# Kernel optimization log

Measured on AMD Instinct MI355X. Metric: run time of the kernel, lower is better.

Reference implementation:

```python
import jax, jax.numpy as jnp
import numpy as np

E = 1024      # embed_dim
QH = 16       # query heads
KVH = 4       # kv heads
HD = E // QH  # head_dim = 64
KVE = HD * KVH  # 256
EPS = 1e-5
ROPE_BASE = 10000.0


def rope(x, d):
    # Faithful to the source RoPE: d == number of heads (x.shape[-2]),
    # and the 'sequence' axis of the cache is x.shape[0] (the batch dim).
    # rope(x) = x*cos + (x*sin) * neg_half(x)  (note: nonlinear in x).
    b = x.shape[0]
    theta = 1.0 / (ROPE_BASE ** (jnp.arange(0, d, 2, dtype=jnp.float32) / d))  # (d//2,)
    seq_idx = jnp.arange(b, dtype=jnp.float32)                                 # (b,)
    idx_theta = seq_idx[:, None] * theta[None, :]                              # (b, d//2)
    idx2 = jnp.concatenate([idx_theta, idx_theta], axis=-1)                    # (b, d)
    # cached shape (b,1,1,d); source permutes (0,1,3,2) -> (b,1,d,1)
    cos = jnp.cos(idx2)[:, None, :, None]  # (b,1,d,1)
    sin = jnp.sin(idx2)[:, None, :, None]
    d2 = d // 2
    # split of the LAST dim (head_dim) at d//2 == num_heads//2, as in source
    neg = jnp.concatenate([-x[..., d2:], x[..., :d2]], axis=-1)
    return x * cos + (x * sin) * neg


def setup_inputs() -> dict:
    key = jax.random.key(0)
    ks = jax.random.split(key, 12)
    b, n = 1, 2048

    def xavier(k, shape):
        fan_out, fan_in = shape
        std = (2.0 / (fan_in + fan_out)) ** 0.5
        return jax.random.normal(k, shape, dtype=jnp.float32) * std

    return {
        "query": jax.random.normal(ks[0], (b, n, E), dtype=jnp.float32),
        "key": jax.random.normal(ks[1], (b, n, E), dtype=jnp.float32),
        "value": jax.random.normal(ks[2], (b, n, E), dtype=jnp.float32),
        "Wq": xavier(ks[3], (E, E)),
        "bq": jnp.zeros((E,), jnp.float32),
        "Wk": xavier(ks[4], (KVE, E)),
        "bk": jnp.zeros((KVE,), jnp.float32),
        "Wv": xavier(ks[5], (KVE, E)),
        "bv": jnp.zeros((KVE,), jnp.float32),
        "gamma": jnp.ones((E,), jnp.float32),
        "beta": jnp.zeros((E,), jnp.float32),
    }


def reference(query, key, value, Wq, bq, Wk, bk, Wv, bv, gamma, beta):
    b, n, _ = query.shape
    q = query @ Wq.T + bq            # (b,n,E)
    k = key @ Wk.T + bk              # (b,n,KVE)
    v = value @ Wv.T + bv            # (b,n,KVE)

    q = q.reshape(b, n, QH, HD)      # b n h d
    k = k.reshape(b, n, KVH, HD)
    v = v.reshape(b, n, KVH, HD)

    q = rope(q, QH)
    k = rope(k, KVH)

    # b n h d -> b h n d
    q = jnp.transpose(q, (0, 2, 1, 3))
    k = jnp.transpose(k, (0, 2, 1, 3))
    v = jnp.transpose(v, (0, 2, 1, 3))

    scale = float(HD) ** 0.5
    q = q / scale

    g = QH // KVH
    # 'b (h g) n d -> b g h n d' : h outer, g inner
    q = q.reshape(b, KVH, g, n, HD)              # (b, h, g, n, d)
    q = jnp.transpose(q, (0, 2, 1, 3, 4))        # (b, g, h, n, d)

    sim = jnp.einsum('bghnd,bhsd->bghns', q, k)  # (b,g,h,n,s)
    attn = jax.nn.softmax(sim, axis=-1)
    out = jnp.einsum('bghns,bhsd->bghnd', attn, v)

    # 'b g h n d -> b n (h g) d'
    out = jnp.transpose(out, (0, 3, 2, 1, 4))    # (b, n, h, g, d)
    x = out.reshape(b, n, QH * HD)               # (b, n, E)

    # LayerNorm (biased variance, as in torch)
    mu = jnp.mean(x, axis=-1, keepdims=True)
    var = jnp.mean((x - mu) ** 2, axis=-1, keepdims=True)
    x = (x - mu) * jax.lax.rsqrt(var + EPS) * gamma + beta

    # NOTE: source computes out_proj(x) but returns x, so out_proj is dead code.
    return x
```

## Files before the change

kernel.cpp:

```cpp
#include <hip/hip_runtime.h>
#include <math.h>

#define EDIM   1024
#define KVEDIM 256
#define HDIM   64
#define QHEADS 16

typedef __attribute__((ext_vector_type(8))) short short8;
typedef __attribute__((ext_vector_type(4))) float f32x4;

__device__ __forceinline__ short f2b(float a) {
    unsigned ua = __builtin_bit_cast(unsigned, a);
    ua += 0x7fffu + ((ua >> 16) & 1u);
    return (short)(ua >> 16);
}
__device__ __forceinline__ unsigned cvtpk(float a, float b) {
    unsigned r;
    asm("v_cvt_pk_bf16_f32 %0, %1, %2" : "=v"(r) : "v"(a), "v"(b));
    return r;
}

__global__ __launch_bounds__(256)
void proj_gemm(const float* __restrict__ Aq, const float* __restrict__ Ak,
               const float* __restrict__ Av,
               const float* __restrict__ Wqf, const float* __restrict__ Wkf,
               const float* __restrict__ Wvf,
               const float* __restrict__ bq, const float* __restrict__ bk,
               const float* __restrict__ bv,
               short* __restrict__ Cq, short* __restrict__ Ck,
               short* __restrict__ Cv, float qscale, int n)
{
    const int bid = blockIdx.x;
    const float* A; const float* W; const float* bias; short* C;
    int N, bm, bn; float scale; int vtrans;
    if (bid < 512) {
        A = Aq; W = Wqf; bias = bq; C = Cq; N = EDIM; scale = qscale; vtrans = 0;
        bm = (bid >> 4) * 64; bn = (bid & 15) * 64;
    } else if (bid < 640) {
        int i = bid - 512;
        A = Ak; W = Wkf; bias = bk; C = Ck; N = KVEDIM; scale = 1.0f; vtrans = 0;
        bm = (i >> 2) * 64; bn = (i & 3) * 64;
    } else {
        int i = bid - 640;
        A = Av; W = Wvf; bias = bv; C = Cv; N = KVEDIM; scale = 1.0f; vtrans = 1;
        bm = (i >> 2) * 64; bn = (i & 3) * 64;
    }
    const int K = EDIM;

    __shared__ short As[64 * 72];
    __shared__ short Ws[64 * 72];

    const int t = threadIdx.x, lane = t & 63, wv = t >> 6;
    const int lm = lane & 15, quad = lane >> 4;
    const int q8 = quad * 8, q4 = quad * 4;
    const int wm = (wv & 1) * 32, wn = (wv >> 1) * 32;
    const int sr = t >> 2, c0 = (t & 3) * 16;

    const f32x4 zero = {0.f, 0.f, 0.f, 0.f};
    f32x4 acc[2][2] = {{zero, zero}, {zero, zero}};

    for (int k0 = 0; k0 < K; k0 += 64) {
        __syncthreads();
        {
            const float4* ap = (const float4*)&A[(size_t)(bm + sr) * K + k0 + c0];
            float4 a0 = ap[0], a1 = ap[1], a2 = ap[2], a3 = ap[3];
            uint4 o0, o1;
            o0.x = cvtpk(a0.x, a0.y); o0.y = cvtpk(a0.z, a0.w);
            o0.z = cvtpk(a1.x, a1.y); o0.w = cvtpk(a1.z, a1.w);
            o1.x = cvtpk(a2.x, a2.y); o1.y = cvtpk(a2.z, a2.w);
            o1.z = cvtpk(a3.x, a3.y); o1.w = cvtpk(a3.z, a3.w);
            *(uint4*)&As[sr * 72 + c0]     = o0;
            *(uint4*)&As[sr * 72 + c0 + 8] = o1;
            const float4* wp = (const float4*)&W[(size_t)(bn + sr) * K + k0 + c0];
            float4 w0 = wp[0], w1 = wp[1], w2 = wp[2], w3 = wp[3];
            uint4 p0, p1;
            p0.x = cvtpk(w0.x, w0.y); p0.y = cvtpk(w0.z, w0.w);
            p0.z = cvtpk(w1.x, w1.y); p0.w = cvtpk(w1.z, w1.w);
            p1.x = cvtpk(w2.x, w2.y); p1.y = cvtpk(w2.z, w2.w);
            p1.z = cvtpk(w3.x, w3.y); p1.w = cvtpk(w3.z, w3.w);
            *(uint4*)&Ws[sr * 72 + c0]     = p0;
            *(uint4*)&Ws[sr * 72 + c0 + 8] = p1;
        }
        __syncthreads();
        #pragma unroll
        for (int ks = 0; ks < 2; ++ks) {
            short8 af[2], bfr[2];
            #pragma unroll
            for (int i = 0; i < 2; ++i)
                af[i] = *(const short8*)&As[(wm + i * 16 + lm) * 72 + ks * 32 + q8];
            #pragma unroll
            for (int j = 0; j < 2; ++j)
                bfr[j] = *(const short8*)&Ws[(wn + j * 16 + lm) * 72 + ks * 32 + q8];
            #pragma unroll
            for (int i = 0; i < 2; ++i)
                #pragma unroll
                for (int j = 0; j < 2; ++j)
                    acc[i][j] = __builtin_amdgcn_mfma_f32_16x16x32_bf16(
                        af[i], bfr[j], acc[i][j], 0, 0, 0);
        }
    }

    if (!vtrans) {
        #pragma unroll
        for (int j = 0; j < 2; ++j) {
            float bj = bias[bn + wn + j * 16 + lm];
            #pragma unroll
            for (int i = 0; i < 2; ++i)
                #pragma unroll
                for (int r = 0; r < 4; ++r)
                    C[(size_t)(bm + wm + i * 16 + q4 + r) * N + bn + wn + j * 16 + lm] =
                        f2b((acc[i][j][r] + bj) * scale);
        }
    } else {
        #pragma unroll
        for (int j = 0; j < 2; ++j) {
            float bj = bias[bn + wn + j * 16 + lm];
            const size_t drow = (size_t)(bn + wn + j * 16 + lm) * n;
            #pragma unroll
            for (int i = 0; i < 2; ++i) {
                uint2 o;
                o.x = cvtpk(acc[i][j][0] + bj, acc[i][j][1] + bj);
                o.y = cvtpk(acc[i][j][2] + bj, acc[i][j][3] + bj);
                *(uint2*)&C[drow + bm + wm + i * 16 + q4] = o;
            }
        }
    }
}

__global__ __launch_bounds__(256, 4)
void attn_mfma(const short* __restrict__ q, const short* __restrict__ k,
               const short* __restrict__ vt, float* __restrict__ x,
               float* __restrict__ opart, float* __restrict__ lpart,
               int n, int s_len, int partial)
{
    __shared__ short Ks[64 * 64];
    __shared__ short Vs[4096];

    const int kvh = blockIdx.y;
    const int r0  = blockIdx.x * 16;
    const int t = threadIdx.x, lane = t & 63, wv = t >> 6;
    const int qh = (kvh << 2) | wv;
    const int lm = lane & 15, quad = lane >> 4, q8 = quad * 8;

    short8 qf0, qf1;
    {
        const short* qp = &q[(size_t)(r0 + lm) * EDIM + qh * HDIM];
        qf0 = *(const short8*)&qp[q8];
        qf1 = *(const short8*)&qp[32 + q8];
    }

    const f32x4 zero = {0.f, 0.f, 0.f, 0.f};
    f32x4 oacc[4] = {zero, zero, zero, zero};
    float lp = 0.f;

    const int sr  = t >> 2;
    const int scs = (t & 3) * 16;
    const int swS = (sr & 7) << 3;
    const int kw0 = sr * 64 + (scs ^ swS);
    const int kw1 = sr * 64 + ((scs + 8) ^ swS);
    const int krx  = q8 ^ ((lm & 7) << 3);
    const int krx2 = (32 + q8) ^ ((lm & 7) << 3);

    const int vd = t >> 2, vc = t & 3;
    const int vktp = vc >> 1, vhalf = vc & 1;
    int vsx[4];
    #pragma unroll
    for (int p = 0; p < 4; ++p) {
        int slot = ((vd >> 4) << 7) + (vktp << 6) + (p << 4) + (vd & 15);
        vsx[p] = slot ^ ((slot >> 4) & 7);
    }

    const int s_lo = (int)blockIdx.z * s_len;
    const int nt = s_len >> 6;
    const short* kb = k + (size_t)kvh * HDIM;
    const short* vb = vt + (size_t)(kvh * HDIM + vd) * n;

    uint4 kra, krb, vra, vrb;
    {
        const uint4* ks = (const uint4*)&kb[(size_t)(s_lo + sr) * KVEDIM + scs];
        kra = ks[0]; krb = ks[1];
        const uint4* vs = (const uint4*)&vb[s_lo + vc * 16];
        vra = vs[0]; vrb = vs[1];
    }

    for (int it = 0; it < nt; ++it) {
        *(uint4*)&Ks[kw0] = kra;
        *(uint4*)&Ks[kw1] = krb;
        {
            uint2 o;
            o.x = vra.x; o.y = vra.y; *(uint2*)&Vs[vsx[0] * 8 + vhalf * 4] = o;
            o.x = vra.z; o.y = vra.w; *(uint2*)&Vs[vsx[1] * 8 + vhalf * 4] = o;
            o.x = vrb.x; o.y = vrb.y; *(uint2*)&Vs[vsx[2] * 8 + vhalf * 4] = o;
            o.x = vrb.z; o.y = vrb.w; *(uint2*)&Vs[vsx[3] * 8 + vhalf * 4] = o;
        }
        __syncthreads();

        if (it + 1 < nt) {
            const int s1 = s_lo + (it + 1) * 64;
            const uint4* ks = (const uint4*)&kb[(size_t)(s1 + sr) * KVEDIM + scs];
            kra = ks[0]; krb = ks[1];
            const uint4* vs = (const uint4*)&vb[s1 + vc * 16];
            vra = vs[0]; vrb = vs[1];
        }

        uint2 pa[4];
        #pragma unroll
        for (int kt = 0; kt < 4; ++kt) {
            const int krow = (kt * 16 + lm) * 64;
            short8 kf0 = *(const short8*)&Ks[krow + krx];
            short8 kf1 = *(const short8*)&Ks[krow + krx2];
            f32x4 s = zero;
            s = __builtin_amdgcn_mfma_f32_16x16x32_bf16(kf0, qf0, s, 0, 0, 0);
            s = __builtin_amdgcn_mfma_f32_16x16x32_bf16(kf1, qf1, s, 0, 0, 0);
            float p0 = exp2f(s[0]), p1 = exp2f(s[1]);
            float p2 = exp2f(s[2]), p3 = exp2f(s[3]);
            lp += (p0 + p1) + (p2 + p3);
            pa[kt].x = cvtpk(p0, p1);
            pa[kt].y = cvtpk(p2, p3);
        }

        uint4 ap0; ap0.x = pa[0].x; ap0.y = pa[0].y; ap0.z = pa[1].x; ap0.w = pa[1].y;
        uint4 ap1; ap1.x = pa[2].x; ap1.y = pa[2].y; ap1.z = pa[3].x; ap1.w = pa[3].y;
        #pragma unroll
        for (int dt = 0; dt < 4; ++dt) {
            int sb0 = dt * 128 + quad * 16 + lm;
            int sx0 = sb0 ^ ((sb0 >> 4) & 7);
            int sb1 = sb0 + 64;
            int sx1 = sb1 ^ ((sb1 >> 4) & 7);
            oacc[dt] = __builtin_amdgcn_mfma_f32_16x16x32_bf16(
                __builtin_bit_cast(short8, ap0),
                *(const short8*)&Vs[sx0 * 8], oacc[dt], 0, 0, 0);
            oacc[dt] = __builtin_amdgcn_mfma_f32_16x16x32_bf16(
                __builtin_bit_cast(short8, ap1),
                *(const short8*)&Vs[sx1 * 8], oacc[dt], 0, 0, 0);
        }
        __syncthreads();
    }

    float lt = lp;
    lt += __shfl_xor(lt, 16);
    lt += __shfl_xor(lt, 32);

    if (partial) {
        float* xp = opart + (size_t)blockIdx.z * n * EDIM;
        if (lane < 16)
            lpart[(size_t)blockIdx.z * n * QHEADS + (size_t)(r0 + lane) * QHEADS + qh] = lt;
        #pragma unroll
        for (int r = 0; r < 4; ++r) {
            const int row = r0 + quad * 4 + r;
            #pragma unroll
            for (int dt = 0; dt < 4; ++dt)
                xp[(size_t)row * EDIM + qh * HDIM + dt * 16 + lm] = oacc[dt][r];
        }
    } else {
        float linv[4];
        #pragma unroll
        for (int r = 0; r < 4; ++r)
            linv[r] = 1.0f / __shfl(lt, quad * 4 + r);
        #pragma unroll
        for (int r = 0; r < 4; ++r) {
            const int row = r0 + quad * 4 + r;
            #pragma unroll
            for (int dt = 0; dt < 4; ++dt)
                x[(size_t)row * EDIM + qh * HDIM + dt * 16 + lm] = oacc[dt][r] * linv[r];
        }
    }
}

__global__ __launch_bounds__(256)
void ln_kernel(float* __restrict__ x, const float* __restrict__ gamma,
               const float* __restrict__ beta,
               const float* __restrict__ opart, const float* __restrict__ lpart,
               int nsplit, int n)
{
    const int row = blockIdx.x;
    const int t = threadIdx.x;

    float4 xv;
    if (nsplit > 0) {
        const int head = t >> 4;
        float l = 0.f;
        float4 s = {0.f, 0.f, 0.f, 0.f};
        for (int z = 0; z < nsplit; ++z) {
            const float4 o = *(const float4*)&opart[(size_t)z * n * EDIM +
                                                    (size_t)row * EDIM + t * 4];
            s.x += o.x; s.y += o.y; s.z += o.z; s.w += o.w;
            l += lpart[(size_t)z * n * QHEADS + (size_t)row * QHEADS + head];
        }
        const float inv = 1.f / l;
        xv.x = s.x * inv; xv.y = s.y * inv; xv.z = s.z * inv; xv.w = s.w * inv;
    } else {
        xv = *(const float4*)&x[(size_t)row * EDIM + t * 4];
    }

    float sm  = xv.x + xv.y + xv.z + xv.w;
    float sq = xv.x * xv.x + xv.y * xv.y + xv.z * xv.z + xv.w * xv.w;
    #pragma unroll
    for (int m = 1; m < 64; m <<= 1) {
        sm += __shfl_xor(sm, m);
        sq += __shfl_xor(sq, m);
    }
    __shared__ float ws_[4], wq_[4];
    const int wave = t >> 6;
    if ((t & 63) == 0) { ws_[wave] = sm; wq_[wave] = sq; }
    __syncthreads();
    sm = ws_[0] + ws_[1] + ws_[2] + ws_[3];
    sq = wq_[0] + wq_[1] + wq_[2] + wq_[3];

    const float mu   = sm * (1.f / EDIM);
    const float var  = sq * (1.f / EDIM) - mu * mu;
    const float rstd = rsqrtf(var + 1e-5f);

    float4 g = *(const float4*)&gamma[t * 4];
    float4 b = *(const float4*)&beta[t * 4];
    float4 o;
    o.x = (xv.x - mu) * rstd * g.x + b.x;
    o.y = (xv.y - mu) * rstd * g.y + b.y;
    o.z = (xv.z - mu) * rstd * g.z + b.z;
    o.w = (xv.w - mu) * rstd * g.w + b.w;
    *(float4*)&x[(size_t)row * EDIM + t * 4] = o;
}

extern "C" void kernel_launch(void* const* d_in, const int* in_sizes, int n_in,
                              void* d_out, int out_size, void* d_ws, size_t ws_size,
                              hipStream_t stream)
{
    const float* query = (const float*)d_in[0];
    const float* key   = (const float*)d_in[1];
    const float* value = (const float*)d_in[2];
    const float* Wq    = (const float*)d_in[3];
    const float* bq    = (const float*)d_in[4];
    const float* Wk    = (const float*)d_in[5];
    const float* bk    = (const float*)d_in[6];
    const float* Wv    = (const float*)d_in[7];
    const float* bv    = (const float*)d_in[8];
    const float* gamma = (const float*)d_in[9];
    const float* beta  = (const float*)d_in[10];
    float* out = (float*)d_out;

    const int n = in_sizes[0] / EDIM;

    short* qb  = (short*)d_ws;
    short* kb  = qb + (size_t)n * EDIM;
    short* vtb = kb + (size_t)n * KVEDIM;
    short* ws_end = vtb + (size_t)KVEDIM * n;

    const size_t base_bytes = (size_t)((char*)ws_end - (char*)d_ws);
    int nsplit = 0;
    for (int cand = 4; cand >= 1; cand >>= 1) {
        if (n % (64 * cand)) continue;
        size_t need = base_bytes +
                      (size_t)cand * ((size_t)n * EDIM + (size_t)n * QHEADS) * sizeof(float);
        if (need <= ws_size) { nsplit = cand; break; }
    }
    float* opart = (float*)ws_end;
    float* lpart = opart + (size_t)(nsplit > 0 ? nsplit : 1) * n * EDIM;

    const float qscale = 0.125f * 1.44269504088896f;

    proj_gemm<<<dim3(768), 256, 0, stream>>>(
        query, key, value, Wq, Wk, Wv, bq, bk, bv, qb, kb, vtb, qscale, n);

    const int zdim  = (nsplit > 0) ? nsplit : 1;
    const int s_len = n / zdim;
    attn_mfma<<<dim3(n / 16, 4, zdim), 256, 0, stream>>>(
        qb, kb, vtb, out, opart, lpart, n, s_len, nsplit > 0 ? 1 : 0);

    ln_kernel<<<dim3(n), 256, 0, stream>>>(out, gamma, beta, opart, lpart, nsplit, n);
}
```

Measured before the change: 155.5 us.

## Process two 16-row query tiles per attention block to reuse K/V tiles

New measurement: 152.7 us (median of 2 runs). About the same (-1.8%).

```diff
diff --git a/kernel.cpp b/kernel.cpp
--- a/kernel.cpp
+++ b/kernel.cpp
@@ -137,21 +137,26 @@
     __shared__ short Vs[4096];
 
     const int kvh = blockIdx.y;
-    const int r0  = blockIdx.x * 16;
+    const int r0  = blockIdx.x * 32;
     const int t = threadIdx.x, lane = t & 63, wv = t >> 6;
     const int qh = (kvh << 2) | wv;
     const int lm = lane & 15, quad = lane >> 4, q8 = quad * 8;
 
-    short8 qf0, qf1;
-    {
-        const short* qp = &q[(size_t)(r0 + lm) * EDIM + qh * HDIM];
-        qf0 = *(const short8*)&qp[q8];
-        qf1 = *(const short8*)&qp[32 + q8];
+    short8 qf[2][2];
+    #pragma unroll
+    for (int qt = 0; qt < 2; ++qt) {
+        const short* qp = &q[(size_t)(r0 + qt * 16 + lm) * EDIM + qh * HDIM];
+        qf[qt][0] = *(const short8*)&qp[q8];
+        qf[qt][1] = *(const short8*)&qp[32 + q8];
     }
 
     const f32x4 zero = {0.f, 0.f, 0.f, 0.f};
-    f32x4 oacc[4] = {zero, zero, zero, zero};
-    float lp = 0.f;
+    f32x4 oacc[2][4];
+    #pragma unroll
+    for (int qt = 0; qt < 2; ++qt)
+        #pragma unroll
+        for (int dt = 0; dt < 4; ++dt) oacc[qt][dt] = zero;
+    float lp[2] = {0.f, 0.f};
 
     const int sr  = t >> 2;
     const int scs = (t & 3) * 16;
@@ -203,66 +208,83 @@
             vra = vs[0]; vrb = vs[1];
         }
 
-        uint2 pa[4];
+        uint2 pa[2][4];
         #pragma unroll
         for (int kt = 0; kt < 4; ++kt) {
             const int krow = (kt * 16 + lm) * 64;
             short8 kf0 = *(const short8*)&Ks[krow + krx];
             short8 kf1 = *(const short8*)&Ks[krow + krx2];
-            f32x4 s = zero;
-            s = __builtin_amdgcn_mfma_f32_16x16x32_bf16(kf0, qf0, s, 0, 0, 0);
-            s = __builtin_amdgcn_mfma_f32_16x16x32_bf16(kf1, qf1, s, 0, 0, 0);
-            float p0 = exp2f(s[0]), p1 = exp2f(s[1]);
-            float p2 = exp2f(s[2]), p3 = exp2f(s[3]);
-            lp += (p0 + p1) + (p2 + p3);
-            pa[kt].x = cvtpk(p0, p1);
-            pa[kt].y = cvtpk(p2, p3);
-        }
-
-        uint4 ap0; ap0.x = pa[0].x; ap0.y = pa[0].y; ap0.z = pa[1].x; ap0.w = pa[1].y;
-        uint4 ap1; ap1.x = pa[2].x; ap1.y = pa[2].y; ap1.z = pa[3].x; ap1.w = pa[3].y;
+            #pragma unroll
+            for (int qt = 0; qt < 2; ++qt) {
+                f32x4 s = zero;
+                s = __builtin_amdgcn_mfma_f32_16x16x32_bf16(kf0, qf[qt][0], s, 0, 0, 0);
+                s = __builtin_amdgcn_mfma_f32_16x16x32_bf16(kf1, qf[qt][1], s, 0, 0, 0);
+                float p0 = exp2f(s[0]), p1 = exp2f(s[1]);
+                float p2 = exp2f(s[2]), p3 = exp2f(s[3]);
+                lp[qt] += (p0 + p1) + (p2 + p3);
+                pa[qt][kt].x = cvtpk(p0, p1);
+                pa[qt][kt].y = cvtpk(p2, p3);
+            }
+        }
+
+        uint4 ap[2][2];
+        #pragma unroll
+        for (int qt = 0; qt < 2; ++qt) {
+            ap[qt][0].x = pa[qt][0].x; ap[qt][0].y = pa[qt][0].y;
+            ap[qt][0].z = pa[qt][1].x; ap[qt][0].w = pa[qt][1].y;
+            ap[qt][1].x = pa[qt][2].x; ap[qt][1].y = pa[qt][2].y;
+            ap[qt][1].z = pa[qt][3].x; ap[qt][1].w = pa[qt][3].y;
+        }
         #pragma unroll
         for (int dt = 0; dt < 4; ++dt) {
             int sb0 = dt * 128 + quad * 16 + lm;
             int sx0 = sb0 ^ ((sb0 >> 4) & 7);
             int sb1 = sb0 + 64;
             int sx1 = sb1 ^ ((sb1 >> 4) & 7);
-            oacc[dt] = __builtin_amdgcn_mfma_f32_16x16x32_bf16(
-                __builtin_bit_cast(short8, ap0),
-                *(const short8*)&Vs[sx0 * 8], oacc[dt], 0, 0, 0);
-            oacc[dt] = __builtin_amdgcn_mfma_f32_16x16x32_bf16(
-                __builtin_bit_cast(short8, ap1),
-                *(const short8*)&Vs[sx1 * 8], oacc[dt], 0, 0, 0);
+            short8 vf0 = *(const short8*)&Vs[sx0 * 8];
+            short8 vf1 = *(const short8*)&Vs[sx1 * 8];
+            #pragma unroll
+            for (int qt = 0; qt < 2; ++qt) {
+                oacc[qt][dt] = __builtin_amdgcn_mfma_f32_16x16x32_bf16(
+                    __builtin_bit_cast(short8, ap[qt][0]), vf0, oacc[qt][dt], 0, 0, 0);
+                oacc[qt][dt] = __builtin_amdgcn_mfma_f32_16x16x32_bf16(
+                    __builtin_bit_cast(short8, ap[qt][1]), vf1, oacc[qt][dt], 0, 0, 0);
+            }
         }
         __syncthreads();
     }
 
-    float lt = lp;
-    lt += __shfl_xor(lt, 16);
-    lt += __shfl_xor(lt, 32);
-
-    if (partial) {
-        float* xp = opart + (size_t)blockIdx.z * n * EDIM;
-        if (lane < 16)
-            lpart[(size_t)blockIdx.z * n * QHEADS + (size_t)(r0 + lane) * QHEADS + qh] = lt;
-        #pragma unroll
-        for (int r = 0; r < 4; ++r) {
-            const int row = r0 + quad * 4 + r;
-            #pragma unroll
-            for (int dt = 0; dt < 4; ++dt)
-                xp[(size_t)row * EDIM + qh * HDIM + dt * 16 + lm] = oacc[dt][r];
-        }
-    } else {
-        float linv[4];
-        #pragma unroll
-        for (int r = 0; r < 4; ++r)
-            linv[r] = 1.0f / __shfl(lt, quad * 4 + r);
-        #pragma unroll
-        for (int r = 0; r < 4; ++r) {
-            const int row = r0 + quad * 4 + r;
-            #pragma unroll
-            for (int dt = 0; dt < 4; ++dt)
-                x[(size_t)row * EDIM + qh * HDIM + dt * 16 + lm] = oacc[dt][r] * linv[r];
+    #pragma unroll
+    for (int qt = 0; qt < 2; ++qt) {
+        float lt = lp[qt];
+        lt += __shfl_xor(lt, 16);
+        lt += __shfl_xor(lt, 32);
+
+        if (partial) {
+            float* xp = opart + (size_t)blockIdx.z * n * EDIM;
+            if (lane < 16)
+                lpart[(size_t)blockIdx.z * n * QHEADS +
+                      (size_t)(r0 + qt * 16 + lane) * QHEADS + qh] = lt;
+            #pragma unroll
+            for (int r = 0; r < 4; ++r) {
+                const int row = r0 + qt * 16 + quad * 4 + r;
+                #pragma unroll
+                for (int dt = 0; dt < 4; ++dt)
+                    xp[(size_t)row * EDIM + qh * HDIM + dt * 16 + lm] = oacc[qt][dt][r];
+            }
+        } else {
+            float linv[4];
+            #pragma unroll
+            for (int r = 0; r < 4; ++r)
+                linv[r] = 1.0f / __shfl(lt, quad * 4 + r);
+            #pragma unroll
+            for (int r = 0; r < 4; ++r) {
+                const int row = r0 + qt * 16 + quad * 4 + r;
+                #pragma unroll
+                for (int dt = 0; dt < 4; ++dt)
+                    x[(size_t)row * EDIM + qh * HDIM + dt * 16 + lm] =
+                        oacc[qt][dt][r] * linv[r];
+            }
         }
     }
 }
@@ -363,7 +385,7 @@
 
     const int zdim  = (nsplit > 0) ? nsplit : 1;
     const int s_len = n / zdim;
-    attn_mfma<<<dim3(n / 16, 4, zdim), 256, 0, stream>>>(
+    attn_mfma<<<dim3(n / 32, 4, zdim), 256, 0, stream>>>(
         qb, kb, vtb, out, opart, lpart, n, s_len, nsplit > 0 ? 1 : 0);
 
     ln_kernel<<<dim3(n), 256, 0, stream>>>(out, gamma, beta, opart, lpart, nsplit, n);
```
